# Performance work log

Measured on AMD Instinct MI355X. Metric: run time of the kernel, lower is better.

The kernel has to match this reference:

```python
import jax, jax.numpy as jnp
import numpy as np

B, T, D, U = 32, 2048, 512, 512

def setup_inputs() -> dict:
    key = jax.random.key(0)
    ks = jax.random.split(key, 8)
    s = 0.02
    return {
        "query": jax.random.normal(ks[0], (B, D), dtype=jnp.float32),
        "values": jax.random.normal(ks[1], (B, T, D), dtype=jnp.float32),
        "W1_w": jax.random.normal(ks[2], (D, U), dtype=jnp.float32) * s,
        "W1_b": jnp.zeros((U,), dtype=jnp.float32),
        "W2_w": jax.random.normal(ks[3], (D, U), dtype=jnp.float32) * s,
        "W2_b": jnp.zeros((U,), dtype=jnp.float32),
        "V_w": jax.random.normal(ks[4], (U, 1), dtype=jnp.float32) * s,
        "V_b": jnp.zeros((1,), dtype=jnp.float32),
    }

def reference(query, values, W1_w, W1_b, W2_w, W2_b, V_w, V_b):
    # query: [B, D] -> [B, 1, U]; values: [B, T, D] -> [B, T, U]
    q_proj = (query @ W1_w + W1_b)[:, None, :]              # [B, 1, U]
    v_proj = jnp.einsum('btd,du->btu', values, W2_w) + W2_b  # [B, T, U]
    score = jnp.tanh(q_proj + v_proj) @ V_w + V_b            # [B, T, 1]
    attn = jax.nn.softmax(score, axis=1)                     # [B, T, 1]
    context = jnp.sum(attn * values, axis=1)                 # [B, D]
    return context, attn
```

## Files before the change

### kernel.cpp

```cpp
#include <hip/hip_runtime.h>
#include <hip/hip_bf16.h>
#include <cstddef>
#include <cstdint>

#define B_ 32
#define T_ 2048
#define D_ 512
#define U_ 512

typedef __attribute__((ext_vector_type(8))) short bf16x8;
typedef __attribute__((ext_vector_type(4))) float f32x4;

__device__ __forceinline__ unsigned short f2bf(float f) {
  union { float f; unsigned u; } x; x.f = f;
  unsigned r = x.u + 0x7fffu + ((x.u >> 16) & 1u);
  return (unsigned short)(r >> 16);
}
__device__ __forceinline__ unsigned pack2bf(float a, float b) {
  return (unsigned)f2bf(a) | ((unsigned)f2bf(b) << 16);
}
__device__ __forceinline__ unsigned pack2bf_fast(float a, float b) {
  union { float f; unsigned u; } xa, xb; xa.f = a; xb.f = b;
  return __builtin_amdgcn_perm(xb.u + 0x8000u, xa.u + 0x8000u, 0x07060302u);
}
__device__ __forceinline__ float tanh_fast(float x) {
  float e = __expf(2.0f * x);
  return 1.0f - 2.0f * __builtin_amdgcn_rcpf(e + 1.0f);
}

#define AS1C(p) ((const __attribute__((address_space(1))) unsigned*)(p))
#define AS3(p)  ((__attribute__((address_space(3))) unsigned*)(p))

__global__ void kA_prep(const float* __restrict__ W2, unsigned* __restrict__ W2P,
                        const float* __restrict__ query, const float* __restrict__ W1,
                        const float* __restrict__ W1b, const float* __restrict__ W2b,
                        float* __restrict__ qp, float* __restrict__ score,
                        float* __restrict__ ctx) {
  const int tid = threadIdx.x;
  if (blockIdx.x < 256) {
    #pragma unroll
    for (int ii = 0; ii < 2; ++ii) {
      int p = blockIdx.x * 512 + ii * 256 + tid;
      int j = (p & 3) * 2;
      int l = (p >> 2) & 63;
      int t = p >> 8;
      int u = (t >> 4) * 16 + (l & 15);
      int k = (t & 15) * 32 + ((l >> 4) << 3) + j;
      W2P[p] = pack2bf(W2[(size_t)k * U_ + u], W2[(size_t)(k + 1) * U_ + u]);
    }
  } else {
    __shared__ float qs[D_];
    const int blk = blockIdx.x - 256;
    const int b = blk >> 1, uhh = (blk & 1) * 256;
    qs[tid] = query[b * D_ + tid];
    qs[tid + 256] = query[b * D_ + tid + 256];
    __syncthreads();
    const int u = uhh + tid;
    float a0 = 0, a1 = 0, a2 = 0, a3 = 0, a4 = 0, a5 = 0, a6 = 0, a7 = 0;
    for (int d = 0; d < D_; d += 8) {
      a0 += qs[d + 0] * W1[(size_t)(d + 0) * U_ + u];
      a1 += qs[d + 1] * W1[(size_t)(d + 1) * U_ + u];
      a2 += qs[d + 2] * W1[(size_t)(d + 2) * U_ + u];
      a3 += qs[d + 3] * W1[(size_t)(d + 3) * U_ + u];
      a4 += qs[d + 4] * W1[(size_t)(d + 4) * U_ + u];
      a5 += qs[d + 5] * W1[(size_t)(d + 5) * U_ + u];
      a6 += qs[d + 6] * W1[(size_t)(d + 6) * U_ + u];
      a7 += qs[d + 7] * W1[(size_t)(d + 7) * U_ + u];
    }
    qp[b * U_ + u] = ((a0 + a1) + (a2 + a3)) + ((a4 + a5) + (a6 + a7)) + W1b[u] + W2b[u];
    const int gt = blk * 256 + tid;
    ctx[gt] = 0.0f;
    #pragma unroll
    for (int i = 0; i < 4; ++i) score[i * 16384 + gt] = 0.0f;
  }
}

__global__ __launch_bounds__(256, 2) void k2_dma(
    const float* __restrict__ values, const unsigned short* __restrict__ W2P,
    const float* __restrict__ qp, const float* __restrict__ Vw,
    float* __restrict__ score) {
  constexpr int GS = 260;
  __shared__ float av[2][16 * GS];
  const int tid = threadIdx.x;
  const int bx = blockIdx.x;
  const int mt = bx >> 1, uh = bx & 1;
  const int m0 = mt * 64;
  const int b = m0 >> 11;
  const int l = tid & 63, w = tid >> 6;
  const int lr = l & 15, lq = l >> 4;

  const int drow = l >> 4;
  const int dcol = (l & 15) * 4;

  f32x4 acc[4][4];
  #pragma unroll
  for (int mi = 0; mi < 4; ++mi)
    #pragma unroll
    for (int ni = 0; ni < 4; ++ni) acc[mi][ni] = (f32x4){0.f, 0.f, 0.f, 0.f};

  const unsigned short* Bb = W2P + (size_t)(uh * 16 + w * 4) * 8192 + (size_t)l * 8;

  auto stage = [&](int e, int p) {
    #pragma unroll
    for (int j = 0; j < 4; ++j) {
      int g = w * 4 + j;
      const float* gp = values + (size_t)(m0 + g * 4 + drow) * D_ + e * 64 + dcol;
      __builtin_amdgcn_global_load_lds(AS1C(gp), AS3(&av[p][g * GS]), 16, 0, 0);
    }
  };

  bf16x8 Bf[2][2][4];
  stage(0, 0);
  #pragma unroll
  for (int kq = 0; kq < 2; ++kq)
    #pragma unroll
    for (int ni = 0; ni < 4; ++ni)
      Bf[0][kq][ni] = *(const bf16x8*)(Bb + (size_t)ni * 8192 + (size_t)kq * 512);

  const int afb = (lr >> 2) * GS + (lr & 3) * 64 + lq * 8;

  for (int e = 0; e < 8; ++e) {
    const int p = e & 1;
    __syncthreads();
    if (e < 7) {
      stage(e + 1, p ^ 1);
      #pragma unroll
      for (int kq = 0; kq < 2; ++kq)
        #pragma unroll
        for (int ni = 0; ni < 4; ++ni)
          Bf[p ^ 1][kq][ni] = *(const bf16x8*)(Bb + (size_t)ni * 8192 + (size_t)(2 * e + 2 + kq) * 512);
    }
    #pragma unroll
    for (int kq = 0; kq < 2; ++kq) {
      bf16x8 a[4];
      #pragma unroll
      for (int mi = 0; mi < 4; ++mi) {
        const float* ap = &av[p][mi * 4 * GS + afb + kq * 32];
        f32x4 f0 = *(const f32x4*)ap;
        f32x4 f1 = *(const f32x4*)(ap + 4);
        unsigned u0 = pack2bf_fast(f0.x, f0.y);
        unsigned u1 = pack2bf_fast(f0.z, f0.w);
        unsigned u2 = pack2bf_fast(f1.x, f1.y);
        unsigned u3 = pack2bf_fast(f1.z, f1.w);
        unsigned au[4] = {u0, u1, u2, u3};
        a[mi] = *(const bf16x8*)au;
      }
      #pragma unroll
      for (int ni = 0; ni < 4; ++ni)
        #pragma unroll
        for (int mi = 0; mi < 4; ++mi)
          acc[mi][ni] = __builtin_amdgcn_mfma_f32_16x16x32_bf16(a[mi], Bf[p][kq][ni], acc[mi][ni], 0, 0, 0);
    }
  }

  float sacc[4][4];
  #pragma unroll
  for (int mi = 0; mi < 4; ++mi)
    #pragma unroll
    for (int r = 0; r < 4; ++r) sacc[mi][r] = 0.0f;
  #pragma unroll
  for (int ni = 0; ni < 4; ++ni) {
    int u = uh * 256 + w * 64 + ni * 16 + lr;
    float qpv = qp[b * U_ + u], vv = Vw[u];
    #pragma unroll
    for (int mi = 0; mi < 4; ++mi)
      #pragma unroll
      for (int r = 0; r < 4; ++r)
        sacc[mi][r] += tanh_fast(acc[mi][ni][r] + qpv) * vv;
  }
  #pragma unroll
  for (int mi = 0; mi < 4; ++mi)
    #pragma unroll
    for (int r = 0; r < 4; ++r) {
      float v = sacc[mi][r];
      v += __shfl_xor(v, 1); v += __shfl_xor(v, 2);
      v += __shfl_xor(v, 4); v += __shfl_xor(v, 8);
      if (lr == 0) atomicAdd(&score[m0 + mi * 16 + lq * 4 + r], v);
    }
}

__global__ void k3_softmax(const float* __restrict__ score, float* __restrict__ attn) {
  __shared__ float red[8];
  const int b = blockIdx.x, tid = threadIdx.x;
  const float* s = score + b * T_;
  float v[8];
  float mx = -1e30f;
  #pragma unroll
  for (int i = 0; i < 8; ++i) { v[i] = s[tid + i * 256]; mx = fmaxf(mx, v[i]); }
  #pragma unroll
  for (int off = 1; off < 64; off <<= 1) mx = fmaxf(mx, __shfl_xor(mx, off));
  if ((tid & 63) == 0) red[tid >> 6] = mx;
  __syncthreads();
  mx = fmaxf(fmaxf(red[0], red[1]), fmaxf(red[2], red[3]));
  float sum = 0.0f;
  #pragma unroll
  for (int i = 0; i < 8; ++i) { v[i] = __expf(v[i] - mx); sum += v[i]; }
  #pragma unroll
  for (int off = 1; off < 64; off <<= 1) sum += __shfl_xor(sum, off);
  if ((tid & 63) == 0) red[4 + (tid >> 6)] = sum;
  __syncthreads();
  sum = (red[4] + red[5]) + (red[6] + red[7]);
  float inv = 1.0f / sum;
  #pragma unroll
  for (int i = 0; i < 8; ++i) attn[b * T_ + tid + i * 256] = v[i] * inv;
}

__global__ void k4_ctx(const float* __restrict__ values, const float* __restrict__ attn,
                       float* __restrict__ ctx) {
  __shared__ float at[64];
  __shared__ float ps[512];
  const int blk = blockIdx.x;
  const int b = blk >> 5, tc = blk & 31;
  const int tid = threadIdx.x;
  if (tid < 64) at[tid] = attn[b * T_ + tc * 64 + tid];
  __syncthreads();
  const int q = tid & 127;
  const int r0 = tid >> 7;
  const float4* vb = (const float4*)(values + ((size_t)b * T_ + tc * 64) * D_);
  float ax = 0.f, ay = 0.f, az = 0.f, aw = 0.f;
  #pragma unroll 8
  for (int tt = 0; tt < 32; ++tt) {
    int row = tt * 2 + r0;
    float4 v = vb[(size_t)row * 128 + q];
    float a = at[row];
    ax += a * v.x; ay += a * v.y; az += a * v.z; aw += a * v.w;
  }
  if (r0 == 1) { ps[4 * q] = ax; ps[4 * q + 1] = ay; ps[4 * q + 2] = az; ps[4 * q + 3] = aw; }
  __syncthreads();
  if (r0 == 0) {
    atomicAdd(&ctx[b * D_ + 4 * q + 0], ax + ps[4 * q + 0]);
    atomicAdd(&ctx[b * D_ + 4 * q + 1], ay + ps[4 * q + 1]);
    atomicAdd(&ctx[b * D_ + 4 * q + 2], az + ps[4 * q + 2]);
    atomicAdd(&ctx[b * D_ + 4 * q + 3], aw + ps[4 * q + 3]);
  }
}

extern "C" void kernel_launch(void* const* d_in, const int* in_sizes, int n_in,
                              void* d_out, int out_size, void* d_ws, size_t ws_size,
                              hipStream_t stream) {
  const float* query = (const float*)d_in[0];
  const float* values = (const float*)d_in[1];
  const float* W1w = (const float*)d_in[2];
  const float* W1b = (const float*)d_in[3];
  const float* W2w = (const float*)d_in[4];
  const float* W2b = (const float*)d_in[5];
  const float* Vw  = (const float*)d_in[6];

  float* out = (float*)d_out;
  float* ctx  = out;
  float* attn = out + B_ * D_;
  float* score = attn;

  char* ws = (char*)d_ws;
  unsigned* W2P = (unsigned*)ws;
  float* qp    = (float*)(ws + 512 * 1024);

  kA_prep<<<320, 256, 0, stream>>>(W2w, W2P, query, W1w, W1b, W2b, qp, score, ctx);
  k2_dma<<<2048, 256, 0, stream>>>(values, (const unsigned short*)W2P, qp, Vw, score);
  k3_softmax<<<32, 256, 0, stream>>>(score, attn);
  k4_ctx<<<1024, 256, 0, stream>>>(values, attn, ctx);
}
```

Baseline: 287.1 us.

## Swizzle LDS layout, shrink B register buffering, raise k2 occupancy to 3

The padded LDS layout for the values tile is replaced with an XOR-swizzled layout of 64 floats per row. The global-to-LDS DMA addresses and the A-fragment reads are permuted to match, so LDS shrinks and bank conflicts are avoided without padding. The double-buffered B fragments (two full K-steps) become a single current/next pair per k-group, which cuts register pressure so launch bounds can request 3 blocks per SIMD. The trade-off is less prefetch distance on the W2 loads and more loop iterations.

```diff
diff --git a/kernel.cpp b/kernel.cpp
--- a/kernel.cpp
+++ b/kernel.cpp
@@ -75,12 +75,11 @@
   }
 }
 
-__global__ __launch_bounds__(256, 2) void k2_dma(
+__global__ __launch_bounds__(256, 3) void k2_dma(
     const float* __restrict__ values, const unsigned short* __restrict__ W2P,
     const float* __restrict__ qp, const float* __restrict__ Vw,
     float* __restrict__ score) {
-  constexpr int GS = 260;
-  __shared__ float av[2][16 * GS];
+  __shared__ float av[2][4096];
   const int tid = threadIdx.x;
   const int bx = blockIdx.x;
   const int mt = bx >> 1, uh = bx & 1;
@@ -90,7 +89,7 @@
   const int lr = l & 15, lq = l >> 4;
 
   const int drow = l >> 4;
-  const int dcol = (l & 15) * 4;
+  const int dchunk = l & 15;
 
   f32x4 acc[4][4];
   #pragma unroll
@@ -104,53 +103,48 @@
     #pragma unroll
     for (int j = 0; j < 4; ++j) {
       int g = w * 4 + j;
-      const float* gp = values + (size_t)(m0 + g * 4 + drow) * D_ + e * 64 + dcol;
-      __builtin_amdgcn_global_load_lds(AS1C(gp), AS3(&av[p][g * GS]), 16, 0, 0);
+      int row = g * 4 + drow;
+      int q = dchunk ^ (row & 15);
+      const float* gp = values + (size_t)(m0 + row) * D_ + e * 64 + q * 4;
+      __builtin_amdgcn_global_load_lds(AS1C(gp), AS3(&av[p][g * 256]), 16, 0, 0);
     }
   };
 
-  bf16x8 Bf[2][2][4];
+  bf16x8 Bc[4], Bn[4];
   stage(0, 0);
   #pragma unroll
-  for (int kq = 0; kq < 2; ++kq)
-    #pragma unroll
-    for (int ni = 0; ni < 4; ++ni)
-      Bf[0][kq][ni] = *(const bf16x8*)(Bb + (size_t)ni * 8192 + (size_t)kq * 512);
-
-  const int afb = (lr >> 2) * GS + (lr & 3) * 64 + lq * 8;
-
-  for (int e = 0; e < 8; ++e) {
-    const int p = e & 1;
-    __syncthreads();
-    if (e < 7) {
-      stage(e + 1, p ^ 1);
-      #pragma unroll
-      for (int kq = 0; kq < 2; ++kq)
-        #pragma unroll
-        for (int ni = 0; ni < 4; ++ni)
-          Bf[p ^ 1][kq][ni] = *(const bf16x8*)(Bb + (size_t)ni * 8192 + (size_t)(2 * e + 2 + kq) * 512);
-    }
-    #pragma unroll
-    for (int kq = 0; kq < 2; ++kq) {
-      bf16x8 a[4];
-      #pragma unroll
-      for (int mi = 0; mi < 4; ++mi) {
-        const float* ap = &av[p][mi * 4 * GS + afb + kq * 32];
-        f32x4 f0 = *(const f32x4*)ap;
-        f32x4 f1 = *(const f32x4*)(ap + 4);
-        unsigned u0 = pack2bf_fast(f0.x, f0.y);
-        unsigned u1 = pack2bf_fast(f0.z, f0.w);
-        unsigned u2 = pack2bf_fast(f1.x, f1.y);
-        unsigned u3 = pack2bf_fast(f1.z, f1.w);
-        unsigned au[4] = {u0, u1, u2, u3};
-        a[mi] = *(const bf16x8*)au;
-      }
+  for (int ni = 0; ni < 4; ++ni) Bc[ni] = *(const bf16x8*)(Bb + (size_t)ni * 8192);
+
+  for (int kg = 0; kg < 16; ++kg) {
+    const int e = kg >> 1, p = e & 1;
+    if ((kg & 1) == 0) {
+      __syncthreads();
+      if (e < 7) stage(e + 1, p ^ 1);
+    }
+    if (kg < 15) {
       #pragma unroll
       for (int ni = 0; ni < 4; ++ni)
-        #pragma unroll
-        for (int mi = 0; mi < 4; ++mi)
-          acc[mi][ni] = __builtin_amdgcn_mfma_f32_16x16x32_bf16(a[mi], Bf[p][kq][ni], acc[mi][ni], 0, 0, 0);
-    }
+        Bn[ni] = *(const bf16x8*)(Bb + (size_t)ni * 8192 + (size_t)(kg + 1) * 512);
+    }
+    const int kq = kg & 1;
+    bf16x8 a[4];
+    #pragma unroll
+    for (int mi = 0; mi < 4; ++mi) {
+      const int row = mi * 16 + lr;
+      const int p0 = (kq * 8 + lq * 2) ^ lr;
+      f32x4 flo = *(const f32x4*)&av[p][row * 64 + (p0 << 2)];
+      f32x4 fhi = *(const f32x4*)&av[p][row * 64 + ((p0 ^ 1) << 2)];
+      unsigned au[4] = { pack2bf_fast(flo.x, flo.y), pack2bf_fast(flo.z, flo.w),
+                         pack2bf_fast(fhi.x, fhi.y), pack2bf_fast(fhi.z, fhi.w) };
+      a[mi] = *(const bf16x8*)au;
+    }
+    #pragma unroll
+    for (int ni = 0; ni < 4; ++ni)
+      #pragma unroll
+      for (int mi = 0; mi < 4; ++mi)
+        acc[mi][ni] = __builtin_amdgcn_mfma_f32_16x16x32_bf16(a[mi], Bc[ni], acc[mi][ni], 0, 0, 0);
+    #pragma unroll
+    for (int ni = 0; ni < 4; ++ni) Bc[ni] = Bn[ni];
   }
 
   float sacc[4][4];
```

Result: faster. 277.9 us (-3.2%).
